# Kernel tuning notes

Measured on AMD Instinct MI355X. Metric: run time of the kernel, lower is better.

## Reference

```python
import jax, jax.numpy as jnp
import numpy as np

IN_CH = 64
HIDDEN_CH = 256

def setup_inputs() -> dict:
    key = jax.random.key(0)
    k = jax.random.split(key, 8)
    za = jax.random.normal(k[0], (8, 256, IN_CH), dtype=jnp.float32)
    zb = jax.random.normal(k[1], (8, 256, IN_CH), dtype=jnp.float32)
    # 1x1 conv weights stored as (out_ch, in_ch); biases zero per torch init
    w0 = jax.random.normal(k[2], (HIDDEN_CH, IN_CH), dtype=jnp.float32) * 0.05
    b0 = jnp.zeros((HIDDEN_CH,), dtype=jnp.float32)
    w1 = jax.random.normal(k[3], (HIDDEN_CH, HIDDEN_CH), dtype=jnp.float32) * 0.05
    b1 = jnp.zeros((HIDDEN_CH,), dtype=jnp.float32)
    w2 = jax.random.normal(k[4], (1, HIDDEN_CH), dtype=jnp.float32) * 0.05
    b2 = jnp.zeros((1,), dtype=jnp.float32)
    return {"za": za, "zb": zb, "w0": w0, "b0": b0, "w1": w1, "b1": b1, "w2": w2, "b2": b2}

def _leaky_relu(x):
    return jnp.where(x >= 0, x, 0.01 * x)  # torch LeakyReLU default slope

def reference(za, zb, w0, b0, w1, b1, w2, b2):
    # z_dif: (N, A, B, C) pairwise broadcast difference (channel-last; 1x1 conv = per-pixel linear)
    z_dif = za[:, :, None, :] - zb[:, None, :, :]
    y = _leaky_relu(jnp.einsum('nabc,hc->nabh', z_dif, w0) + b0)
    y = _leaky_relu(jnp.einsum('nabh,gh->nabg', y, w1) + b1)
    y = jax.nn.sigmoid(jnp.einsum('nabh,oh->nabo', y, w2) + b2)
    return y[..., 0]  # (N, A, B)
```

## Files before the change

### kernel.cpp

```cpp
#include <hip/hip_runtime.h>
#include <hip/hip_fp16.h>


typedef float f32x16 __attribute__((ext_vector_type(16)));
typedef _Float16 f16x8 __attribute__((ext_vector_type(8)));
typedef int i32x4 __attribute__((ext_vector_type(4)));

__global__ __launch_bounds__(256) void pack_all(
    const float* __restrict__ za, const float* __restrict__ zb,
    const float* __restrict__ w0, const float* __restrict__ b0,
    const float* __restrict__ w1,
    _Float16* __restrict__ upack, _Float16* __restrict__ vpack,
    _Float16* __restrict__ vlin, _Float16* __restrict__ w1pk) {
  int bid = blockIdx.x;
  int tid = threadIdx.x;
  if (bid < 2048) {
    int nr = bid;
    int n = nr >> 8, r = nr & 255;
    __shared__ float arow[64], brow[64];
    if (tid < 64) arow[tid] = za[nr * 64 + tid];
    else if (tid < 128) brow[tid - 64] = zb[nr * 64 + (tid - 64)];
    __syncthreads();
    int h = tid;
    const float* w0r = w0 + h * 64;
    float ua = 0.f, vb = 0.f;
#pragma unroll
    for (int c = 0; c < 64; c += 4) {
      float4 w = *reinterpret_cast<const float4*>(w0r + c);
      ua += w.x * arow[c] + w.y * arow[c + 1] + w.z * arow[c + 2] + w.w * arow[c + 3];
      vb += w.x * brow[c] + w.y * brow[c + 1] + w.z * brow[c + 2] + w.w * brow[c + 3];
    }
    upack[nr * 256 + h] = (_Float16)(ua + b0[h]);
    _Float16 vh = (_Float16)vb;
    vlin[nr * 256 + h] = vh;
    int bblk = r >> 5, lcol = r & 31;
    int kiter = h >> 4, rem = h & 15, lh = rem >> 3, j = rem & 7;
    int lane = lh * 32 + lcol;
    vpack[(((n * 8 + bblk) * 16 + kiter) * 64 + lane) * 8 + j] = vh;
  } else {
    int id = (bid - 2048) * 256 + tid;
    int g = id >> 8, k = id & 255;
    int gt = g >> 5, lcol = g & 31;
    int kiter = k >> 4, rem = k & 15, lh = rem >> 3, j = rem & 7;
    int lane = lh * 32 + lcol;
    w1pk[((kiter * 8 + gt) * 64 + lane) * 8 + j] = (_Float16)(0.495f * w1[id]);
  }
}

__global__ __launch_bounds__(256) void pq_kernel(
    const _Float16* __restrict__ upack, const _Float16* __restrict__ vlin,
    const float* __restrict__ w1, const float* __restrict__ b1,
    float* __restrict__ Ra, float* __restrict__ Sb) {
  int bid = blockIdx.x;
  int which = bid >> 9;
  int nr0 = (bid & 511) * 4;
  __shared__ float rows[4][256];
  int tid = threadIdx.x;
  const _Float16* src = which ? vlin : upack;
#pragma unroll
  for (int i = 0; i < 4; ++i)
    rows[i][tid] = (float)src[(size_t)(nr0 + i) * 256 + tid];
  __syncthreads();
  int g = tid;
  const float* w1r = w1 + (size_t)g * 256;
  float acc0 = 0.f, acc1 = 0.f, acc2 = 0.f, acc3 = 0.f;
#pragma unroll 8
  for (int k = 0; k < 256; k += 4) {
    float4 w = *reinterpret_cast<const float4*>(w1r + k);
    acc0 += w.x * rows[0][k] + w.y * rows[0][k + 1] + w.z * rows[0][k + 2] + w.w * rows[0][k + 3];
    acc1 += w.x * rows[1][k] + w.y * rows[1][k + 1] + w.z * rows[1][k + 2] + w.w * rows[1][k + 3];
    acc2 += w.x * rows[2][k] + w.y * rows[2][k + 1] + w.z * rows[2][k + 2] + w.w * rows[2][k + 3];
    acc3 += w.x * rows[3][k] + w.y * rows[3][k + 1] + w.z * rows[3][k + 2] + w.w * rows[3][k + 3];
  }
  if (which == 0) {
    float bb = b1[g];
    Ra[(size_t)(nr0 + 0) * 256 + g] = 0.505f * acc0 + bb;
    Ra[(size_t)(nr0 + 1) * 256 + g] = 0.505f * acc1 + bb;
    Ra[(size_t)(nr0 + 2) * 256 + g] = 0.505f * acc2 + bb;
    Ra[(size_t)(nr0 + 3) * 256 + g] = 0.505f * acc3 + bb;
  } else {
    Sb[(size_t)(nr0 + 0) * 256 + g] = 0.505f * acc0;
    Sb[(size_t)(nr0 + 1) * 256 + g] = 0.505f * acc1;
    Sb[(size_t)(nr0 + 2) * 256 + g] = 0.505f * acc2;
    Sb[(size_t)(nr0 + 3) * 256 + g] = 0.505f * acc3;
  }
}

__global__ __launch_bounds__(512, 2) void fused_main(
    const _Float16* __restrict__ upack, const _Float16* __restrict__ vpack,
    const _Float16* __restrict__ w1pk,
    const float* __restrict__ Ra, const float* __restrict__ Sb,
    const float* __restrict__ w2, const float* __restrict__ b2,
    float* __restrict__ out) {
  __shared__ float lds_p[2][8][32];
  int bid = blockIdx.x;
  int n = bid >> 5;
  int bblk = (bid >> 2) & 7;
  int aq = bid & 3;
  int tid = threadIdx.x;
  int ws = tid >> 6;
  int l = tid & 63;
  int l31 = l & 31, lh = l >> 5;

  f16x8 w1f[16];
#pragma unroll
  for (int kt = 0; kt < 16; ++kt)
    w1f[kt] = *reinterpret_cast<const f16x8*>(w1pk + ((kt * 8 + ws) * 64 + l) * 8);

  const _Float16* vbase = vpack + (size_t)((n * 8 + bblk) * 16) * 512 + l * 8;
  f16x8 vf[16];
#pragma unroll
  for (int kt = 0; kt < 16; ++kt)
    vf[kt] = *reinterpret_cast<const f16x8*>(vbase + kt * 512);

  float sbf[16], w2f[16];
  const float* sbrow = Sb + (size_t)(n * 256 + bblk * 32 + l31) * 256;
#pragma unroll
  for (int rg = 0; rg < 4; ++rg) {
    int gbase = ws * 32 + 8 * rg + 4 * lh;
    float4 ss = *reinterpret_cast<const float4*>(sbrow + gbase);
    float4 ww = *reinterpret_cast<const float4*>(w2 + gbase);
    sbf[4 * rg + 0] = ss.x; sbf[4 * rg + 1] = ss.y;
    sbf[4 * rg + 2] = ss.z; sbf[4 * rg + 3] = ss.w;
    w2f[4 * rg + 0] = ww.x; w2f[4 * rg + 1] = ww.y;
    w2f[4 * rg + 2] = ww.z; w2f[4 * rg + 3] = ww.w;
  }
  float b2v = b2[0];

  const _Float16* ub = upack + (size_t)(n * 256 + aq * 64) * 256 + lh * 8;
  const float* rabase = Ra + (size_t)(n * 256 + aq * 64) * 256;

  for (int it = 0; it < 64; ++it) {
    const _Float16* ur = ub + (size_t)it * 256;
    const float* rar = rabase + (size_t)it * 256;

    f32x16 accA, accB;
#pragma unroll
    for (int rg = 0; rg < 4; ++rg) {
      float4 rr = *reinterpret_cast<const float4*>(rar + ws * 32 + 8 * rg + 4 * lh);
      accA[4 * rg + 0] = rr.x - sbf[4 * rg + 0];
      accA[4 * rg + 1] = rr.y - sbf[4 * rg + 1];
      accA[4 * rg + 2] = rr.z - sbf[4 * rg + 2];
      accA[4 * rg + 3] = rr.w - sbf[4 * rg + 3];
    }
#pragma unroll
    for (int r = 0; r < 16; ++r) accB[r] = 0.f;

#pragma unroll
    for (int kt = 0; kt < 16; ++kt) {
      f16x8 uu = *reinterpret_cast<const f16x8*>(ur + kt * 16);
      f16x8 d = uu - vf[kt];
      i32x4 di = __builtin_bit_cast(i32x4, d);
      di &= 0x7fff7fff;
      f16x8 ad = __builtin_bit_cast(f16x8, di);
      if (kt & 1)
        accB = __builtin_amdgcn_mfma_f32_32x32x16_f16(w1f[kt], ad, accB, 0, 0, 0);
      else
        accA = __builtin_amdgcn_mfma_f32_32x32x16_f16(w1f[kt], ad, accA, 0, 0, 0);
    }

    float p = 0.f;
#pragma unroll
    for (int r = 0; r < 16; ++r) {
      float s = accA[r] + accB[r];
      float h = fmaxf(s, 0.01f * s);
      p = fmaf(h, w2f[r], p);
    }
    p += __shfl_xor(p, 32, 64);

    int ph = it & 1;
    if (l < 32) lds_p[ph][ws][l] = p;
    __syncthreads();
    if (ws == 0 && l < 32) {
      float s = b2v;
#pragma unroll
      for (int w = 0; w < 8; ++w) s += lds_p[ph][w][l];
      int a = aq * 64 + it;
      out[(size_t)(n * 256 + a) * 256 + bblk * 32 + l] = 1.f / (1.f + __expf(-s));
    }
  }
}

extern "C" void kernel_launch(void* const* d_in, const int* in_sizes, int n_in,
                              void* d_out, int out_size, void* d_ws, size_t ws_size,
                              hipStream_t stream) {
  const float* za = (const float*)d_in[0];
  const float* zb = (const float*)d_in[1];
  const float* w0 = (const float*)d_in[2];
  const float* b0 = (const float*)d_in[3];
  const float* w1 = (const float*)d_in[4];
  const float* b1 = (const float*)d_in[5];
  const float* w2 = (const float*)d_in[6];
  const float* b2 = (const float*)d_in[7];
  float* out = (float*)d_out;

  char* ws = (char*)d_ws;
  _Float16* upack = (_Float16*)ws;
  _Float16* vpack = (_Float16*)(ws + (1u << 20));
  _Float16* vlin  = (_Float16*)(ws + (2u << 20));
  _Float16* w1pk  = (_Float16*)(ws + (3u << 20));
  float*    Ra    = (float*)(ws + (7u << 19));
  float*    Sb    = (float*)(ws + (11u << 19));

  pack_all<<<2304, 256, 0, stream>>>(za, zb, w0, b0, w1, upack, vpack, vlin, w1pk);
  pq_kernel<<<1024, 256, 0, stream>>>(upack, vlin, w1, b1, Ra, Sb);
  fused_main<<<256, 512, 0, stream>>>(upack, vpack, w1pk, Ra, Sb, w2, b2, out);
}
```

Measured before the change: 196.0 us.

## Remove per-row block barrier by spilling wave partials and reducing in separate kernel

The main kernel no longer synchronizes all 8 waves after every output row to sum per-wave partial dot products. Each wave instead writes its partials to a global workspace, and a new reduce kernel sums them and applies the bias and sigmoid. If the workspace is too small, a fallback path batches 4 rows per barrier using a larger LDS buffer. This trades 64 block barriers per block for about 16 MB of extra global writes and reads plus an extra kernel launch.

Measured after the change: 177.7 us. 1.1x faster.

```diff
diff --git a/kernel.cpp b/kernel.cpp
--- a/kernel.cpp
+++ b/kernel.cpp
@@ -86,13 +86,13 @@
   }
 }
 
+template <int MODE>
 __global__ __launch_bounds__(512, 2) void fused_main(
     const _Float16* __restrict__ upack, const _Float16* __restrict__ vpack,
     const _Float16* __restrict__ w1pk,
     const float* __restrict__ Ra, const float* __restrict__ Sb,
     const float* __restrict__ w2, const float* __restrict__ b2,
-    float* __restrict__ out) {
-  __shared__ float lds_p[2][8][32];
+    float* __restrict__ pws, float* __restrict__ out) {
   int bid = blockIdx.x;
   int n = bid >> 5;
   int bblk = (bid >> 2) & 7;
@@ -130,55 +130,116 @@
   const _Float16* ub = upack + (size_t)(n * 256 + aq * 64) * 256 + lh * 8;
   const float* rabase = Ra + (size_t)(n * 256 + aq * 64) * 256;
 
-  for (int it = 0; it < 64; ++it) {
-    const _Float16* ur = ub + (size_t)it * 256;
-    const float* rar = rabase + (size_t)it * 256;
-
-    f32x16 accA, accB;
-#pragma unroll
-    for (int rg = 0; rg < 4; ++rg) {
-      float4 rr = *reinterpret_cast<const float4*>(rar + ws * 32 + 8 * rg + 4 * lh);
-      accA[4 * rg + 0] = rr.x - sbf[4 * rg + 0];
-      accA[4 * rg + 1] = rr.y - sbf[4 * rg + 1];
-      accA[4 * rg + 2] = rr.z - sbf[4 * rg + 2];
-      accA[4 * rg + 3] = rr.w - sbf[4 * rg + 3];
+  if constexpr (MODE == 0) {
+    float* pw = pws + ((size_t)bid * 64 * 8 + ws) * 32;
+    for (int it = 0; it < 64; ++it) {
+      const _Float16* ur = ub + (size_t)it * 256;
+      const float* rar = rabase + (size_t)it * 256;
+
+      f32x16 accA, accB;
+#pragma unroll
+      for (int rg = 0; rg < 4; ++rg) {
+        float4 rr = *reinterpret_cast<const float4*>(rar + ws * 32 + 8 * rg + 4 * lh);
+        accA[4 * rg + 0] = rr.x - sbf[4 * rg + 0];
+        accA[4 * rg + 1] = rr.y - sbf[4 * rg + 1];
+        accA[4 * rg + 2] = rr.z - sbf[4 * rg + 2];
+        accA[4 * rg + 3] = rr.w - sbf[4 * rg + 3];
+      }
+#pragma unroll
+      for (int r = 0; r < 16; ++r) accB[r] = 0.f;
+
+#pragma unroll
+      for (int kt = 0; kt < 16; ++kt) {
+        f16x8 uu = *reinterpret_cast<const f16x8*>(ur + kt * 16);
+        f16x8 d = uu - vf[kt];
+        i32x4 di = __builtin_bit_cast(i32x4, d);
+        di &= 0x7fff7fff;
+        f16x8 ad = __builtin_bit_cast(f16x8, di);
+        if (kt & 1)
+          accB = __builtin_amdgcn_mfma_f32_32x32x16_f16(w1f[kt], ad, accB, 0, 0, 0);
+        else
+          accA = __builtin_amdgcn_mfma_f32_32x32x16_f16(w1f[kt], ad, accA, 0, 0, 0);
+      }
+
+      float p = 0.f;
+#pragma unroll
+      for (int r = 0; r < 16; ++r) {
+        float s = accA[r] + accB[r];
+        float h = fmaxf(s, 0.01f * s);
+        p = fmaf(h, w2f[r], p);
+      }
+      p += __shfl_xor(p, 32, 64);
+      if (l < 32) pw[(size_t)it * 256 + l31] = p;
     }
-#pragma unroll
-    for (int r = 0; r < 16; ++r) accB[r] = 0.f;
-
-#pragma unroll
-    for (int kt = 0; kt < 16; ++kt) {
-      f16x8 uu = *reinterpret_cast<const f16x8*>(ur + kt * 16);
-      f16x8 d = uu - vf[kt];
-      i32x4 di = __builtin_bit_cast(i32x4, d);
-      di &= 0x7fff7fff;
-      f16x8 ad = __builtin_bit_cast(f16x8, di);
-      if (kt & 1)
-        accB = __builtin_amdgcn_mfma_f32_32x32x16_f16(w1f[kt], ad, accB, 0, 0, 0);
-      else
-        accA = __builtin_amdgcn_mfma_f32_32x32x16_f16(w1f[kt], ad, accA, 0, 0, 0);
+  } else {
+    __shared__ float lds_p[2][4][8][32];
+    for (int bt = 0; bt < 16; ++bt) {
+      int ph = bt & 1;
+      for (int j = 0; j < 4; ++j) {
+        int it = bt * 4 + j;
+        const _Float16* ur = ub + (size_t)it * 256;
+        const float* rar = rabase + (size_t)it * 256;
+
+        f32x16 accA, accB;
+#pragma unroll
+        for (int rg = 0; rg < 4; ++rg) {
+          float4 rr = *reinterpret_cast<const float4*>(rar + ws * 32 + 8 * rg + 4 * lh);
+          accA[4 * rg + 0] = rr.x - sbf[4 * rg + 0];
+          accA[4 * rg + 1] = rr.y - sbf[4 * rg + 1];
+          accA[4 * rg + 2] = rr.z - sbf[4 * rg + 2];
+          accA[4 * rg + 3] = rr.w - sbf[4 * rg + 3];
+        }
+#pragma unroll
+        for (int r = 0; r < 16; ++r) accB[r] = 0.f;
+
+#pragma unroll
+        for (int kt = 0; kt < 16; ++kt) {
+          f16x8 uu = *reinterpret_cast<const f16x8*>(ur + kt * 16);
+          f16x8 d = uu - vf[kt];
+          i32x4 di = __builtin_bit_cast(i32x4, d);
+          di &= 0x7fff7fff;
+          f16x8 ad = __builtin_bit_cast(f16x8, di);
+          if (kt & 1)
+            accB = __builtin_amdgcn_mfma_f32_32x32x16_f16(w1f[kt], ad, accB, 0, 0, 0);
+          else
+            accA = __builtin_amdgcn_mfma_f32_32x32x16_f16(w1f[kt], ad, accA, 0, 0, 0);
+        }
+
+        float p = 0.f;
+#pragma unroll
+        for (int r = 0; r < 16; ++r) {
+          float s = accA[r] + accB[r];
+          float h = fmaxf(s, 0.01f * s);
+          p = fmaf(h, w2f[r], p);
+        }
+        p += __shfl_xor(p, 32, 64);
+        if (l < 32) lds_p[ph][j][ws][l31] = p;
+      }
+      __syncthreads();
+      if (tid < 128) {
+        int al = tid >> 5, b = tid & 31;
+        float s = b2v;
+#pragma unroll
+        for (int w = 0; w < 8; ++w) s += lds_p[ph][al][w][b];
+        int a = aq * 64 + bt * 4 + al;
+        out[(size_t)(n * 256 + a) * 256 + bblk * 32 + b] = 1.f / (1.f + __expf(-s));
+      }
     }
-
-    float p = 0.f;
-#pragma unroll
-    for (int r = 0; r < 16; ++r) {
-      float s = accA[r] + accB[r];
-      float h = fmaxf(s, 0.01f * s);
-      p = fmaf(h, w2f[r], p);
-    }
-    p += __shfl_xor(p, 32, 64);
-
-    int ph = it & 1;
-    if (l < 32) lds_p[ph][ws][l] = p;
-    __syncthreads();
-    if (ws == 0 && l < 32) {
-      float s = b2v;
-#pragma unroll
-      for (int w = 0; w < 8; ++w) s += lds_p[ph][w][l];
-      int a = aq * 64 + it;
-      out[(size_t)(n * 256 + a) * 256 + bblk * 32 + l] = 1.f / (1.f + __expf(-s));
-    }
-  }
+  }
+}
+
+__global__ __launch_bounds__(256) void reduce_kernel(
+    const float* __restrict__ pws, const float* __restrict__ b2,
+    float* __restrict__ out) {
+  int o = blockIdx.x * 256 + threadIdx.x;
+  int n = o >> 16, a = (o >> 8) & 255, b = o & 255;
+  int bblk = b >> 5, b32 = b & 31, aq = a >> 6, it = a & 63;
+  int mbid = (n << 5) | (bblk << 2) | aq;
+  const float* p = pws + (((size_t)mbid * 64 + it) * 8) * 32 + b32;
+  float s = b2[0];
+#pragma unroll
+  for (int w = 0; w < 8; ++w) s += p[w * 32];
+  out[o] = 1.f / (1.f + __expf(-s));
 }
 
 extern "C" void kernel_launch(void* const* d_in, const int* in_sizes, int n_in,
@@ -201,8 +262,16 @@
   _Float16* w1pk  = (_Float16*)(ws + (3u << 20));
   float*    Ra    = (float*)(ws + (7u << 19));
   float*    Sb    = (float*)(ws + (11u << 19));
+  float*    pws   = (float*)(ws + (15u << 19));
 
   pack_all<<<2304, 256, 0, stream>>>(za, zb, w0, b0, w1, upack, vpack, vlin, w1pk);
   pq_kernel<<<1024, 256, 0, stream>>>(upack, vlin, w1, b1, Ra, Sb);
-  fused_main<<<256, 512, 0, stream>>>(upack, vpack, w1pk, Ra, Sb, w2, b2, out);
-}
+
+  const size_t need = (15ull << 19) + 256ull * 64 * 8 * 32 * 4;
+  if (ws_size >= need) {
+    fused_main<0><<<256, 512, 0, stream>>>(upack, vpack, w1pk, Ra, Sb, w2, b2, pws, out);
+    reduce_kernel<<<2048, 256, 0, stream>>>(pws, b2, out);
+  } else {
+    fused_main<1><<<256, 512, 0, stream>>>(upack, vpack, w1pk, Ra, Sb, w2, b2, nullptr, out);
+  }
+}
```
